# Kernel tuning notes

Measured on AMD Instinct MI355X. Metric: run time of the kernel, lower is better.

## Reference

```python
import jax, jax.numpy as jnp
import numpy as np

B, N, M, T = 64, 1024, 32, 25
R, SO, SA, H, OD = 512, 512, 256, 8, 10

def _ln(x, g, b):
    mu = x.mean(-1, keepdims=True)
    v = ((x - mu) ** 2).mean(-1, keepdims=True)
    return (x - mu) / jnp.sqrt(v + 1e-5) * g + b

def _glu(x):
    a, g = jnp.split(x, 2, axis=-1)
    return a * jax.nn.sigmoid(g)

def setup_inputs() -> dict:
    key = jax.random.key(0)
    ks = jax.random.split(key, 64)
    it = iter(range(64))
    def rn(shape, s=0.05):
        return jax.random.normal(ks[next(it)], shape, jnp.float32) * s
    def zr(shape):
        return jnp.zeros(shape, jnp.float32)
    def on(shape):
        return jnp.ones(shape, jnp.float32)
    inp = dict(
        x=jax.random.normal(ks[next(it)], (B, 1, 28, 28), jnp.float32),
        start_activated_state=rn((N,)),
        start_trace=rn((N, M)),
        ie_w1=rn((128, 784)), ie_b1=zr(128), ie_g1=on(128), ie_bn1=zr(128),
        ie_w2=rn((64, 128)), ie_b2=zr(64), ie_g2=on(64), ie_bn2=zr(64),
        ie_w3=rn((R, 64)), ie_b3=zr(R),
        kv_w=rn((R, R)), kv_b=zr(R), kv_g=on(R), kv_bn=zr(R),
        q_w=rn((R, SA)), q_b=zr(R),
        in_proj_w=rn((3 * R, R)), in_proj_b=zr(3 * R),
        out_proj_w=rn((R, R)), out_proj_b=zr(R),
        syn_w=rn((2 * N, R + N)), syn_b=zr(2 * N), syn_g=on(N), syn_bn=zr(N),
        nlm_w1=rn((N, M, 256)), nlm_b1=zr((N, 256)),
        nlm_w2=rn((N, 128)), nlm_b2=zr(N),
        decay_action=zr(SA), decay_out=zr(SO),
        op_w1=rn((256, SO)), op_b1=zr(256), op_g1=on(256), op_bn1=zr(256),
        op_w2=rn((64, 256)), op_b2=zr(64), op_g2=on(64), op_bn2=zr(64),
        op_w3=rn((OD, 64)), op_b3=zr(OD),
        idx_out_l=jax.random.randint(ks[next(it)], (SO,), 0, N, jnp.int32),
        idx_out_r=jax.random.randint(ks[next(it)], (SO,), 0, N, jnp.int32),
        idx_act_l=jax.random.randint(ks[next(it)], (SA,), 0, N, jnp.int32),
        idx_act_r=jax.random.randint(ks[next(it)], (SA,), 0, N, jnp.int32),
    )
    return inp

def reference(x, start_activated_state, start_trace,
              ie_w1, ie_b1, ie_g1, ie_bn1, ie_w2, ie_b2, ie_g2, ie_bn2, ie_w3, ie_b3,
              kv_w, kv_b, kv_g, kv_bn, q_w, q_b,
              in_proj_w, in_proj_b, out_proj_w, out_proj_b,
              syn_w, syn_b, syn_g, syn_bn,
              nlm_w1, nlm_b1, nlm_w2, nlm_b2,
              decay_action, decay_out,
              op_w1, op_b1, op_g1, op_bn1, op_w2, op_b2, op_g2, op_bn2, op_w3, op_b3,
              idx_out_l, idx_out_r, idx_act_l, idx_act_r):
    Bx = x.shape[0]
    f = x.reshape(Bx, -1)  # [B,784]
    h = jax.nn.relu(_ln(f @ ie_w1.T + ie_b1, ie_g1, ie_bn1))
    h = jax.nn.relu(_ln(h @ ie_w2.T + ie_b2, ie_g2, ie_bn2))
    enc = h @ ie_w3.T + ie_b3                       # [B,R]
    kv = _ln(enc @ kv_w.T + kv_b, kv_g, kv_bn)      # [B,R]; single kv token
    # MultiheadAttention with kv_len == 1: softmax over a single key is exactly 1,
    # so attn_out = out_proj(Wv @ kv + bv) regardless of the query (q_proj of
    # sync_action has no effect on the output). Hoisted out of the tick loop.
    Wv = in_proj_w[2 * R:]
    bv = in_proj_b[2 * R:]
    attn_out = (kv @ Wv.T + bv) @ out_proj_w.T + out_proj_b  # [B,R]
    rA = jnp.exp(-jnp.clip(decay_action, 0.0, 15.0))  # [SA]
    rO = jnp.exp(-jnp.clip(decay_out, 0.0, 15.0))     # [SO]
    act0 = jnp.broadcast_to(start_activated_state, (Bx, N))
    trace0 = jnp.broadcast_to(start_trace, (Bx, N, M))
    # pre-loop 'out' sync init: alpha = z_i*z_j, beta = 1
    aO0 = act0[:, idx_out_l] * act0[:, idx_out_r]
    bO0 = jnp.ones_like(aO0)
    # 'action' sync starts from None; recurrence from (0,0) reproduces it exactly
    aA0 = jnp.zeros((Bx, SA), x.dtype)
    bA0 = jnp.zeros((Bx, SA), x.dtype)
    log_od = np.log(float(OD)).astype(np.float32)

    def step(carry, _):
        trace, act, aA, bA, aO, bO = carry
        ppA = act[:, idx_act_l] * act[:, idx_act_r]
        aA = rA * aA + ppA
        bA = rA * bA + 1.0
        # sync_action -> q_proj -> attention query: no effect on output (see above)
        pre = jnp.concatenate([attn_out, act], axis=-1)          # [B,R+N]
        ns = _ln(_glu(pre @ syn_w.T + syn_b), syn_g, syn_bn)     # [B,N]
        trace = jnp.concatenate([trace[:, :, 1:], ns[:, :, None]], axis=-1)  # [B,N,M]
        # batched per-neuron NLMs: Linear(M,256) -> GLU -> Linear(128,1)
        hh = _glu(jnp.einsum('bnm,nmh->bnh', trace, nlm_w1) + nlm_b1)  # [B,N,128]
        act = jnp.einsum('bnh,nh->bn', hh, nlm_w2) + nlm_b2            # [B,N]
        ppO = act[:, idx_out_l] * act[:, idx_out_r]
        aO = rO * aO + ppO
        bO = rO * bO + 1.0
        syncO = aO / jnp.sqrt(bO + 1e-8)
        p = jax.nn.relu(_ln(syncO @ op_w1.T + op_b1, op_g1, op_bn1))
        p = jax.nn.relu(_ln(p @ op_w2.T + op_b2, op_g2, op_bn2))
        pred = p @ op_w3.T + op_b3                                # [B,OD]
        probs = jax.nn.softmax(pred, axis=-1)
        ent = -jnp.sum(probs * jnp.log(probs + 1e-10), axis=-1) / log_od
        cert = jnp.stack([ent, 1.0 - ent], axis=-1)               # [B,2]
        return (trace, act, aA, bA, aO, bO), (pred, cert)

    _, (preds, certs) = jax.lax.scan(step, (trace0, act0, aA0, bA0, aO0, bO0), None, length=T)
    predictions = jnp.moveaxis(preds, 0, -1)   # [B,OD,T]
    certainties = jnp.moveaxis(certs, 0, -1)   # [B,2,T]
    return predictions, certainties
```

## Files before the change

### kernel.cpp

```cpp
#include <hip/hip_runtime.h>
#include <math.h>

#define TRW 57
#define TRN (TRW * 64)

__device__ __forceinline__ float wave_sum(float v) {
  #pragma unroll
  for (int off = 32; off; off >>= 1) v += __shfl_xor(v, off, 64);
  return v;
}

template<int NT>
__device__ __forceinline__ float2 block_sum2(float a, float b, float2* sh) {
  constexpr int NW = NT / 64;
  a = wave_sum(a); b = wave_sum(b);
  int w = threadIdx.x >> 6, l = threadIdx.x & 63;
  if (l == 0) sh[w] = make_float2(a, b);
  __syncthreads();
  float2 r = make_float2(0.f, 0.f);
  #pragma unroll
  for (int i = 0; i < NW; i++) { r.x += sh[i].x; r.y += sh[i].y; }
  __syncthreads();
  return r;
}

__device__ __forceinline__ float sigmoidf(float x) {
  return 1.f / (1.f + expf(-x));
}

__global__ __launch_bounds__(512) void k_enc(const float* __restrict__ x,
    const float* __restrict__ w1, const float* __restrict__ b1,
    const float* __restrict__ g1, const float* __restrict__ bn1,
    const float* __restrict__ w2, const float* __restrict__ b2,
    const float* __restrict__ g2, const float* __restrict__ bn2,
    const float* __restrict__ w3, const float* __restrict__ b3,
    const float* __restrict__ kvw, const float* __restrict__ kvb,
    const float* __restrict__ kvg, const float* __restrict__ kvbn,
    const float* __restrict__ ipw, const float* __restrict__ ipb,
    const float* __restrict__ opw, const float* __restrict__ opb,
    float* __restrict__ attn) {
  int b = blockIdx.x, tid = threadIdx.x, w = tid >> 6, l = tid & 63;
  __shared__ float xs[784];
  __shared__ float A[512];
  __shared__ float Bv[512];
  __shared__ float buf1[128];
  __shared__ float buf2[64];
  __shared__ float2 sh[8];
  for (int i = tid; i < 784; i += 512) xs[i] = x[b * 784 + i];
  __syncthreads();
  for (int r = 0; r < 16; r++) {
    int o = r * 8 + w;
    float s = 0.f;
    for (int k = l; k < 784; k += 64) s += xs[k] * w1[o * 784 + k];
    s = wave_sum(s);
    if (l == 0) buf1[o] = s + b1[o];
  }
  __syncthreads();
  {
    float v = (tid < 128) ? buf1[tid] : 0.f;
    float2 s2 = block_sum2<512>(v, v * v, sh);
    if (tid < 128) {
      float mu = s2.x * (1.f / 128.f), var = s2.y * (1.f / 128.f) - mu * mu;
      buf1[tid] = fmaxf((v - mu) * rsqrtf(var + 1e-5f) * g1[tid] + bn1[tid], 0.f);
    }
  }
  __syncthreads();
  for (int r = 0; r < 8; r++) {
    int o = r * 8 + w;
    float s = buf1[l] * w2[o * 128 + l] + buf1[l + 64] * w2[o * 128 + l + 64];
    s = wave_sum(s);
    if (l == 0) buf2[o] = s + b2[o];
  }
  __syncthreads();
  if (tid < 64) {
    float v = buf2[tid];
    float sa = wave_sum(v), sb = wave_sum(v * v);
    float mu = sa * (1.f / 64.f), var = sb * (1.f / 64.f) - mu * mu;
    buf2[tid] = fmaxf((v - mu) * rsqrtf(var + 1e-5f) * g2[tid] + bn2[tid], 0.f);
  }
  __syncthreads();
  for (int r = 0; r < 64; r++) {
    int o = r * 8 + w;
    float s = wave_sum(buf2[l] * w3[o * 64 + l]);
    if (l == 0) A[o] = s + b3[o];
  }
  __syncthreads();
  for (int r = 0; r < 64; r++) {
    int o = r * 8 + w;
    float s = 0.f;
    #pragma unroll
    for (int k = 0; k < 8; k++) s += A[l + 64 * k] * kvw[o * 512 + l + 64 * k];
    s = wave_sum(s);
    if (l == 0) Bv[o] = s + kvb[o];
  }
  __syncthreads();
  {
    float v = Bv[tid];
    float2 s2 = block_sum2<512>(v, v * v, sh);
    float mu = s2.x * (1.f / 512.f), var = s2.y * (1.f / 512.f) - mu * mu;
    Bv[tid] = (v - mu) * rsqrtf(var + 1e-5f) * kvg[tid] + kvbn[tid];
  }
  __syncthreads();
  for (int r = 0; r < 64; r++) {
    int o = r * 8 + w;
    float s = 0.f;
    #pragma unroll
    for (int k = 0; k < 8; k++) s += Bv[l + 64 * k] * ipw[(1024 + o) * 512 + l + 64 * k];
    s = wave_sum(s);
    if (l == 0) A[o] = s + ipb[1024 + o];
  }
  __syncthreads();
  for (int r = 0; r < 64; r++) {
    int o = r * 8 + w;
    float s = 0.f;
    #pragma unroll
    for (int k = 0; k < 8; k++) s += A[l + 64 * k] * opw[o * 512 + l + 64 * k];
    s = wave_sum(s);
    if (l == 0) attn[b * 512 + o] = s + opb[o];
  }
}

__global__ void k_setup(const float* __restrict__ st, const float* __restrict__ sas,
                        const int* __restrict__ il, const int* __restrict__ ir,
                        const float* __restrict__ opw1, const float* __restrict__ opw2,
                        float* __restrict__ trace, float* __restrict__ act,
                        float* __restrict__ aO, float* __restrict__ bO,
                        float* __restrict__ w1t, float* __restrict__ w2t) {
  long i = (long)blockIdx.x * 256 + threadIdx.x;
  if (i < 2097152) {
    int b = (int)(i & 63), j = (int)((i >> 6) & 31), n = (int)(i >> 11);
    trace[n * TRN + j * 64 + b] = st[n * 32 + j];
    return;
  }
  i -= 2097152;
  if (i < 65536) {
    act[i] = sas[i & 1023];
    return;
  }
  i -= 65536;
  if (i < 32768) {
    int o = (int)(i & 511);
    aO[i] = sas[il[o]] * sas[ir[o]];
    bO[i] = 1.f;
    return;
  }
  i -= 32768;
  if (i < 131072) {
    int o = (int)(i & 255), k = (int)(i >> 8);
    w1t[i] = opw1[o * 512 + k];
    return;
  }
  i -= 131072;
  if (i < 16384) {
    int o = (int)(i & 63), k = (int)(i >> 6);
    w2t[i] = opw2[o * 256 + k];
  }
}

__device__ void op_body(int b, int t, const float* __restrict__ act,
                        const float* __restrict__ decay,
                        const int* __restrict__ il, const int* __restrict__ ir,
                        float* __restrict__ aO, float* __restrict__ bO,
                        const float* __restrict__ w1t, const float* __restrict__ bb1,
                        const float* __restrict__ g1, const float* __restrict__ bn1,
                        const float* __restrict__ w2t, const float* __restrict__ bb2,
                        const float* __restrict__ g2, const float* __restrict__ bn2,
                        const float* __restrict__ w3, const float* __restrict__ bb3,
                        float* __restrict__ out,
                        float* so, float* p1s, float* qred, float* p2s,
                        float* preds, float2* sh) {
  int tid = threadIdx.x;
  #pragma unroll
  for (int r = 0; r < 2; r++) {
    int o = r * 256 + tid;
    float rr = expf(-fminf(fmaxf(decay[o], 0.f), 15.f));
    float pp = act[b * 1024 + il[o]] * act[b * 1024 + ir[o]];
    float a = rr * aO[b * 512 + o] + pp;
    float bbv = rr * bO[b * 512 + o] + 1.f;
    aO[b * 512 + o] = a;
    bO[b * 512 + o] = bbv;
    so[o] = a * rsqrtf(bbv + 1e-8f);
  }
  __syncthreads();
  float p = bb1[tid];
  #pragma unroll 8
  for (int k = 0; k < 512; k++) p += so[k] * w1t[k * 256 + tid];
  float2 s = block_sum2<256>(p, p * p, sh);
  {
    float mu = s.x * (1.f / 256.f), var = s.y * (1.f / 256.f) - mu * mu;
    p1s[tid] = fmaxf((p - mu) * rsqrtf(var + 1e-5f) * g1[tid] + bn1[tid], 0.f);
  }
  __syncthreads();
  {
    int o = tid & 63, tg = tid >> 6;
    float q = 0.f;
    #pragma unroll 4
    for (int j = 0; j < 64; j++) {
      int k = tg * 64 + j;
      q += p1s[k] * w2t[k * 64 + o];
    }
    qred[tid] = q;
  }
  __syncthreads();
  if (tid < 64) {
    float p2 = qred[tid] + qred[tid + 64] + qred[tid + 128] + qred[tid + 192] + bb2[tid];
    float sa = wave_sum(p2), sb = wave_sum(p2 * p2);
    float mu = sa * (1.f / 64.f), var = sb * (1.f / 64.f) - mu * mu;
    float y = (p2 - mu) * rsqrtf(var + 1e-5f) * g2[tid] + bn2[tid];
    p2s[tid] = fmaxf(y, 0.f);
  }
  __syncthreads();
  if (tid < 160) {
    int o = tid >> 4, j = tid & 15;
    const float* w3r = w3 + o * 64 + j * 4;
    const float* pp2 = p2s + j * 4;
    float sv = w3r[0] * pp2[0] + w3r[1] * pp2[1] + w3r[2] * pp2[2] + w3r[3] * pp2[3];
    #pragma unroll
    for (int off = 8; off; off >>= 1) sv += __shfl_xor(sv, off, 64);
    if (j == 0) {
      float pr = sv + bb3[o];
      preds[o] = pr;
      out[b * 250 + o * 25 + t] = pr;
    }
  }
  __syncthreads();
  if (tid == 0) {
    float mx = preds[0];
    #pragma unroll
    for (int k = 1; k < 10; k++) mx = fmaxf(mx, preds[k]);
    float sum = 0.f, e[10];
    #pragma unroll
    for (int k = 0; k < 10; k++) { e[k] = expf(preds[k] - mx); sum += e[k]; }
    float ent = 0.f;
    #pragma unroll
    for (int k = 0; k < 10; k++) {
      float pr = e[k] / sum;
      ent -= pr * logf(pr + 1e-10f);
    }
    ent *= (1.f / 2.302585093f);
    out[16000 + b * 50 + t] = ent;
    out[16000 + b * 50 + 25 + t] = 1.f - ent;
  }
}

__global__ __launch_bounds__(256) void k_F(const float* __restrict__ attn,
    const float* __restrict__ act, const float* __restrict__ synw,
    float* __restrict__ part,
    const float* __restrict__ decay, const int* __restrict__ il, const int* __restrict__ ir,
    float* __restrict__ aO, float* __restrict__ bO,
    const float* __restrict__ w1t, const float* __restrict__ bb1,
    const float* __restrict__ g1, const float* __restrict__ bn1,
    const float* __restrict__ w2t, const float* __restrict__ bb2,
    const float* __restrict__ g2, const float* __restrict__ bn2,
    const float* __restrict__ w3, const float* __restrict__ bb3,
    float* __restrict__ out, int t) {
  __shared__ __align__(16) float pre_t[32 * 68];
  __shared__ __align__(16) float w_lds[32 * 68];
  __shared__ __align__(16) float so[512];
  __shared__ float p1s[256];
  __shared__ float qred[256];
  __shared__ float p2s[64];
  __shared__ float preds[10];
  __shared__ float2 sh[4];
  int bid = blockIdx.x;
  if (bid >= 512) {
    if (t > 0)
      op_body(bid - 512, t - 1, act, decay, il, ir, aO, bO, w1t, bb1, g1, bn1,
              w2t, bb2, g2, bn2, w3, bb3, out, so, p1s, qred, p2s, preds, sh);
    return;
  }
  int ct = bid & 31;
  int kc = bid >> 5;
  int tid = threadIdx.x;
  int tb = tid >> 4, tc = tid & 15;
  int b0 = tb * 4, c0 = tc * 4;
  float acc[4][4];
  #pragma unroll
  for (int i = 0; i < 4; i++)
    #pragma unroll
    for (int j = 0; j < 4; j++) acc[i][j] = 0.f;

  for (int kt = 0; kt < 96; kt += 32) {
    int k0 = kc * 96 + kt;
    #pragma unroll
    for (int r = 0; r < 8; r++) {
      int idx = r * 256 + tid;
      int kk = idx & 31;
      int bb = idx >> 5;
      int kg = k0 + kk;
      float pv = (kg < 512) ? attn[bb * 512 + kg] : act[bb * 1024 + (kg - 512)];
      pre_t[kk * 68 + bb] = pv;
      w_lds[kk * 68 + bb] = synw[(ct * 64 + bb) * 1536 + kg];
    }
    __syncthreads();
    #pragma unroll 8
    for (int kk = 0; kk < 32; kk++) {
      float4 av = *(const float4*)(pre_t + kk * 68 + b0);
      float4 wv = *(const float4*)(w_lds + kk * 68 + c0);
      float a[4] = {av.x, av.y, av.z, av.w};
      float w[4] = {wv.x, wv.y, wv.z, wv.w};
      #pragma unroll
      for (int i = 0; i < 4; i++)
        #pragma unroll
        for (int j = 0; j < 4; j++) acc[i][j] += a[i] * w[j];
    }
    __syncthreads();
  }
  float* pb = part + kc * (64 * 2048);
  #pragma unroll
  for (int i = 0; i < 4; i++) {
    float4 st4 = make_float4(acc[i][0], acc[i][1], acc[i][2], acc[i][3]);
    *(float4*)(pb + (b0 + i) * 2048 + ct * 64 + c0) = st4;
  }
}

__global__ __launch_bounds__(256) void k_op_tail(const float* __restrict__ act,
    const float* __restrict__ decay, const int* __restrict__ il, const int* __restrict__ ir,
    float* __restrict__ aO, float* __restrict__ bO,
    const float* __restrict__ w1t, const float* __restrict__ bb1,
    const float* __restrict__ g1, const float* __restrict__ bn1,
    const float* __restrict__ w2t, const float* __restrict__ bb2,
    const float* __restrict__ g2, const float* __restrict__ bn2,
    const float* __restrict__ w3, const float* __restrict__ bb3,
    float* __restrict__ out) {
  __shared__ __align__(16) float so[512];
  __shared__ float p1s[256];
  __shared__ float qred[256];
  __shared__ float p2s[64];
  __shared__ float preds[10];
  __shared__ float2 sh[4];
  op_body(blockIdx.x, 24, act, decay, il, ir, aO, bO, w1t, bb1, g1, bn1,
          w2t, bb2, g2, bn2, w3, bb3, out, so, p1s, qred, p2s, preds, sh);
}

__global__ __launch_bounds__(1024) void k_syn_ln(const float* __restrict__ part,
                                                 const float* __restrict__ synb,
                                                 const float* __restrict__ sg,
                                                 const float* __restrict__ sbn,
                                                 float* __restrict__ ns) {
  __shared__ float2 sh[16];
  int b = blockIdx.x, n = threadIdx.x;
  float a = synb[n], g = synb[n + 1024];
  #pragma unroll
  for (int kc = 0; kc < 16; kc++) {
    const float* pb = part + kc * (64 * 2048) + b * 2048;
    a += pb[n];
    g += pb[n + 1024];
  }
  float val = a * sigmoidf(g);
  float2 s = block_sum2<1024>(val, val * val, sh);
  float mu = s.x * (1.f / 1024.f);
  float var = s.y * (1.f / 1024.f) - mu * mu;
  ns[b * 1024 + n] = (val - mu) * rsqrtf(var + 1e-5f) * sg[n] + sbn[n];
}

__global__ __launch_bounds__(256) void k_nlm(const float* __restrict__ trace_c,
                                             float* __restrict__ trace,
                                             const float* __restrict__ ns,
                                             const float* __restrict__ w1,
                                             const float* __restrict__ b1,
                                             const float* __restrict__ w2,
                                             const float* __restrict__ b2,
                                             float* __restrict__ act, int t) {
  int n = blockIdx.x;
  int tid = threadIdx.x;
  int tb = tid >> 5;
  int tjj = tid & 31;
  __shared__ __align__(16) float At[32 * 68];
  __shared__ __align__(16) float w1s[32 * 256];
  __shared__ float b1s[256];
  __shared__ float w2s[128];

  const float4* tw4 = (const float4*)(trace_c + n * TRN + (t + 1) * 64);
  #pragma unroll
  for (int r = 0; r < 2; r++) {
    int idx = r * 256 + tid;
    if (idx < 496) {
      float4 f4 = tw4[idx];
      int fo = idx * 4;
      int m = fo >> 6, bb = fo & 63;
      *(float4*)(At + m * 68 + bb) = f4;
    }
  }
  if (tid < 64) {
    float v = ns[tid * 1024 + n];
    At[31 * 68 + tid] = v;
    trace[n * TRN + (32 + t) * 64 + tid] = v;
  }
  const float4* w1n = (const float4*)(w1 + n * 8192);
  float4* w1s4 = (float4*)w1s;
  #pragma unroll
  for (int r = 0; r < 8; r++) w1s4[r * 256 + tid] = w1n[r * 256 + tid];
  b1s[tid] = b1[n * 256 + tid];
  if (tid < 128) w2s[tid] = w2[n * 128 + tid];
  __syncthreads();

  float h[8][8];
  #pragma unroll
  for (int jj = 0; jj < 8; jj++) {
    float bv = b1s[tjj + 32 * jj];
    #pragma unroll
    for (int i = 0; i < 8; i++) h[i][jj] = bv;
  }
  for (int m = 0; m < 32; m++) {
    float4 a0 = *(const float4*)(At + m * 68 + tb * 8);
    float4 a1 = *(const float4*)(At + m * 68 + tb * 8 + 4);
    float a[8] = {a0.x, a0.y, a0.z, a0.w, a1.x, a1.y, a1.z, a1.w};
    float w[8];
    #pragma unroll
    for (int jj = 0; jj < 8; jj++) w[jj] = w1s[m * 256 + tjj + 32 * jj];
    #pragma unroll
    for (int i = 0; i < 8; i++)
      #pragma unroll
      for (int jj = 0; jj < 8; jj++) h[i][jj] += a[i] * w[jj];
  }
  float b2n = b2[n];
  #pragma unroll
  for (int i = 0; i < 8; i++) {
    float p = 0.f;
    #pragma unroll
    for (int jj = 0; jj < 4; jj++) {
      float hh = h[i][jj] * sigmoidf(h[i][jj + 4]);
      p += hh * w2s[tjj + 32 * jj];
    }
    #pragma unroll
    for (int off = 16; off > 0; off >>= 1) p += __shfl_xor(p, off, 64);
    if (tjj == 0) act[(tb * 8 + i) * 1024 + n] = p + b2n;
  }
}

extern "C" void kernel_launch(void* const* d_in, const int* in_sizes, int n_in,
                              void* d_out, int out_size, void* d_ws, size_t ws_size,
                              hipStream_t stream) {
  const float* x        = (const float*)d_in[0];
  const float* sas      = (const float*)d_in[1];
  const float* st       = (const float*)d_in[2];
  const float* ie_w1    = (const float*)d_in[3];
  const float* ie_b1    = (const float*)d_in[4];
  const float* ie_g1    = (const float*)d_in[5];
  const float* ie_bn1   = (const float*)d_in[6];
  const float* ie_w2    = (const float*)d_in[7];
  const float* ie_b2    = (const float*)d_in[8];
  const float* ie_g2    = (const float*)d_in[9];
  const float* ie_bn2   = (const float*)d_in[10];
  const float* ie_w3    = (const float*)d_in[11];
  const float* ie_b3    = (const float*)d_in[12];
  const float* kv_w     = (const float*)d_in[13];
  const float* kv_b     = (const float*)d_in[14];
  const float* kv_g     = (const float*)d_in[15];
  const float* kv_bn    = (const float*)d_in[16];
  const float* ip_w     = (const float*)d_in[19];
  const float* ip_b     = (const float*)d_in[20];
  const float* op_w     = (const float*)d_in[21];
  const float* op_b     = (const float*)d_in[22];
  const float* syn_w    = (const float*)d_in[23];
  const float* syn_b    = (const float*)d_in[24];
  const float* syn_g    = (const float*)d_in[25];
  const float* syn_bn   = (const float*)d_in[26];
  const float* nlm_w1   = (const float*)d_in[27];
  const float* nlm_b1   = (const float*)d_in[28];
  const float* nlm_w2   = (const float*)d_in[29];
  const float* nlm_b2   = (const float*)d_in[30];
  const float* decay_o  = (const float*)d_in[32];
  const float* op_w1    = (const float*)d_in[33];
  const float* op_b1    = (const float*)d_in[34];
  const float* op_g1    = (const float*)d_in[35];
  const float* op_bn1   = (const float*)d_in[36];
  const float* op_w2    = (const float*)d_in[37];
  const float* op_b2    = (const float*)d_in[38];
  const float* op_g2    = (const float*)d_in[39];
  const float* op_bn2   = (const float*)d_in[40];
  const float* op_w3    = (const float*)d_in[41];
  const float* op_b3    = (const float*)d_in[42];
  const int* idx_ol     = (const int*)d_in[43];
  const int* idx_or     = (const int*)d_in[44];

  float* out = (float*)d_out;
  float* ws = (float*)d_ws;
  float* attn  = ws;
  float* act   = attn + 32768;
  float* aO    = act + 65536;
  float* bO    = aO + 32768;
  float* ns    = bO + 32768;
  float* w1t   = ns + 65536;
  float* w2t   = w1t + 131072;
  float* part  = w2t + 16384;
  float* trace = part + 2097152;

  k_enc<<<64, 512, 0, stream>>>(x, ie_w1, ie_b1, ie_g1, ie_bn1,
                                ie_w2, ie_b2, ie_g2, ie_bn2, ie_w3, ie_b3,
                                kv_w, kv_b, kv_g, kv_bn, ip_w, ip_b, op_w, op_b, attn);
  k_setup<<<9152, 256, 0, stream>>>(st, sas, idx_ol, idx_or, op_w1, op_w2,
                                    trace, act, aO, bO, w1t, w2t);

  for (int t = 0; t < 25; t++) {
    k_F<<<576, 256, 0, stream>>>(attn, act, syn_w, part,
                                 decay_o, idx_ol, idx_or, aO, bO,
                                 w1t, op_b1, op_g1, op_bn1,
                                 w2t, op_b2, op_g2, op_bn2,
                                 op_w3, op_b3, out, t);
    k_syn_ln<<<64, 1024, 0, stream>>>(part, syn_b, syn_g, syn_bn, ns);
    k_nlm<<<1024, 256, 0, stream>>>(trace, trace, ns, nlm_w1, nlm_b1,
                                    nlm_w2, nlm_b2, act, t);
  }
  k_op_tail<<<64, 256, 0, stream>>>(act, decay_o, idx_ol, idx_or, aO, bO,
                                    w1t, op_b1, op_g1, op_bn1,
                                    w2t, op_b2, op_g2, op_bn2,
                                    op_w3, op_b3, out);
}
```

Before: 1.944 ms.

## Transpose encoder weights in setup and compute one output per thread

k_setup now also transposes the input-encoder, kv, value-projection and out-projection weights into a k-blocked float4 layout, stored in the scratch buffer that k_F later reuses. k_enc is rewritten so each thread computes one output neuron with coalesced float4 weight loads and inputs broadcast from shared memory. This replaces the old wave-per-output dot products with their shuffle reductions. The cost is extra transpose work and weight traffic in setup, and k_enc must now run after k_setup.

Result: faster. 1.714 ms (-11.8%).

```diff
diff --git a/kernel.cpp b/kernel.cpp
--- a/kernel.cpp
+++ b/kernel.cpp
@@ -29,103 +29,134 @@
 }
 
 __global__ __launch_bounds__(512) void k_enc(const float* __restrict__ x,
-    const float* __restrict__ w1, const float* __restrict__ b1,
+    const float* __restrict__ w1te, const float* __restrict__ b1,
     const float* __restrict__ g1, const float* __restrict__ bn1,
-    const float* __restrict__ w2, const float* __restrict__ b2,
+    const float* __restrict__ w2te, const float* __restrict__ b2,
     const float* __restrict__ g2, const float* __restrict__ bn2,
-    const float* __restrict__ w3, const float* __restrict__ b3,
-    const float* __restrict__ kvw, const float* __restrict__ kvb,
+    const float* __restrict__ w3te, const float* __restrict__ b3,
+    const float* __restrict__ kvwt, const float* __restrict__ kvb,
     const float* __restrict__ kvg, const float* __restrict__ kvbn,
-    const float* __restrict__ ipw, const float* __restrict__ ipb,
-    const float* __restrict__ opw, const float* __restrict__ opb,
+    const float* __restrict__ vwt, const float* __restrict__ ipb,
+    const float* __restrict__ opwt, const float* __restrict__ opb,
     float* __restrict__ attn) {
-  int b = blockIdx.x, tid = threadIdx.x, w = tid >> 6, l = tid & 63;
+  int b = blockIdx.x, tid = threadIdx.x;
   __shared__ float xs[784];
-  __shared__ float A[512];
-  __shared__ float Bv[512];
-  __shared__ float buf1[128];
-  __shared__ float buf2[64];
+  __shared__ float h1[128];
+  __shared__ float h2[64];
+  __shared__ float enc[512];
+  __shared__ float red[512];
   __shared__ float2 sh[8];
   for (int i = tid; i < 784; i += 512) xs[i] = x[b * 784 + i];
   __syncthreads();
-  for (int r = 0; r < 16; r++) {
-    int o = r * 8 + w;
-    float s = 0.f;
-    for (int k = l; k < 784; k += 64) s += xs[k] * w1[o * 784 + k];
-    s = wave_sum(s);
-    if (l == 0) buf1[o] = s + b1[o];
-  }
-  __syncthreads();
-  {
-    float v = (tid < 128) ? buf1[tid] : 0.f;
-    float2 s2 = block_sum2<512>(v, v * v, sh);
+  {
+    int tg = tid >> 7, o = tid & 127;
+    const float4* wp = (const float4*)w1te;
+    float s0 = 0.f, s1 = 0.f, s2 = 0.f, s3 = 0.f;
+    int kb0 = tg * 49;
+    #pragma unroll 7
+    for (int j = 0; j < 49; j++) {
+      int kb = kb0 + j;
+      float4 w4 = wp[kb * 128 + o];
+      int k = kb * 4;
+      s0 += xs[k] * w4.x; s1 += xs[k + 1] * w4.y;
+      s2 += xs[k + 2] * w4.z; s3 += xs[k + 3] * w4.w;
+    }
+    red[tid] = (s0 + s1) + (s2 + s3);
+    __syncthreads();
+    float v = 0.f;
+    if (tid < 128)
+      v = red[tid] + red[tid + 128] + red[tid + 256] + red[tid + 384] + b1[tid];
+    float2 s2v = block_sum2<512>(tid < 128 ? v : 0.f, tid < 128 ? v * v : 0.f, sh);
     if (tid < 128) {
-      float mu = s2.x * (1.f / 128.f), var = s2.y * (1.f / 128.f) - mu * mu;
-      buf1[tid] = fmaxf((v - mu) * rsqrtf(var + 1e-5f) * g1[tid] + bn1[tid], 0.f);
-    }
-  }
-  __syncthreads();
-  for (int r = 0; r < 8; r++) {
-    int o = r * 8 + w;
-    float s = buf1[l] * w2[o * 128 + l] + buf1[l + 64] * w2[o * 128 + l + 64];
-    s = wave_sum(s);
-    if (l == 0) buf2[o] = s + b2[o];
+      float mu = s2v.x * (1.f / 128.f), var = s2v.y * (1.f / 128.f) - mu * mu;
+      h1[tid] = fmaxf((v - mu) * rsqrtf(var + 1e-5f) * g1[tid] + bn1[tid], 0.f);
+    }
   }
   __syncthreads();
   if (tid < 64) {
-    float v = buf2[tid];
-    float sa = wave_sum(v), sb = wave_sum(v * v);
+    const float4* wp = (const float4*)w2te;
+    float s0 = 0.f, s1 = 0.f, s2 = 0.f, s3 = 0.f;
+    #pragma unroll 8
+    for (int kb = 0; kb < 32; kb++) {
+      float4 w4 = wp[kb * 64 + tid];
+      int k = kb * 4;
+      s0 += h1[k] * w4.x; s1 += h1[k + 1] * w4.y;
+      s2 += h1[k + 2] * w4.z; s3 += h1[k + 3] * w4.w;
+    }
+    float s = (s0 + s1) + (s2 + s3) + b2[tid];
+    float sa = wave_sum(s), sb = wave_sum(s * s);
     float mu = sa * (1.f / 64.f), var = sb * (1.f / 64.f) - mu * mu;
-    buf2[tid] = fmaxf((v - mu) * rsqrtf(var + 1e-5f) * g2[tid] + bn2[tid], 0.f);
-  }
-  __syncthreads();
-  for (int r = 0; r < 64; r++) {
-    int o = r * 8 + w;
-    float s = wave_sum(buf2[l] * w3[o * 64 + l]);
-    if (l == 0) A[o] = s + b3[o];
-  }
-  __syncthreads();
-  for (int r = 0; r < 64; r++) {
-    int o = r * 8 + w;
-    float s = 0.f;
-    #pragma unroll
-    for (int k = 0; k < 8; k++) s += A[l + 64 * k] * kvw[o * 512 + l + 64 * k];
-    s = wave_sum(s);
-    if (l == 0) Bv[o] = s + kvb[o];
-  }
-  __syncthreads();
-  {
-    float v = Bv[tid];
-    float2 s2 = block_sum2<512>(v, v * v, sh);
-    float mu = s2.x * (1.f / 512.f), var = s2.y * (1.f / 512.f) - mu * mu;
-    Bv[tid] = (v - mu) * rsqrtf(var + 1e-5f) * kvg[tid] + kvbn[tid];
-  }
-  __syncthreads();
-  for (int r = 0; r < 64; r++) {
-    int o = r * 8 + w;
-    float s = 0.f;
-    #pragma unroll
-    for (int k = 0; k < 8; k++) s += Bv[l + 64 * k] * ipw[(1024 + o) * 512 + l + 64 * k];
-    s = wave_sum(s);
-    if (l == 0) A[o] = s + ipb[1024 + o];
-  }
-  __syncthreads();
-  for (int r = 0; r < 64; r++) {
-    int o = r * 8 + w;
-    float s = 0.f;
-    #pragma unroll
-    for (int k = 0; k < 8; k++) s += A[l + 64 * k] * opw[o * 512 + l + 64 * k];
-    s = wave_sum(s);
-    if (l == 0) attn[b * 512 + o] = s + opb[o];
+    h2[tid] = fmaxf((s - mu) * rsqrtf(var + 1e-5f) * g2[tid] + bn2[tid], 0.f);
+  }
+  __syncthreads();
+  {
+    const float4* wp = (const float4*)w3te;
+    float s0 = 0.f, s1 = 0.f, s2 = 0.f, s3 = 0.f;
+    #pragma unroll 8
+    for (int kb = 0; kb < 16; kb++) {
+      float4 w4 = wp[kb * 512 + tid];
+      int k = kb * 4;
+      s0 += h2[k] * w4.x; s1 += h2[k + 1] * w4.y;
+      s2 += h2[k + 2] * w4.z; s3 += h2[k + 3] * w4.w;
+    }
+    enc[tid] = (s0 + s1) + (s2 + s3) + b3[tid];
+  }
+  __syncthreads();
+  {
+    const float4* wp = (const float4*)kvwt;
+    float s0 = 0.f, s1 = 0.f, s2 = 0.f, s3 = 0.f;
+    #pragma unroll 8
+    for (int kb = 0; kb < 128; kb++) {
+      float4 w4 = wp[kb * 512 + tid];
+      int k = kb * 4;
+      s0 += enc[k] * w4.x; s1 += enc[k + 1] * w4.y;
+      s2 += enc[k + 2] * w4.z; s3 += enc[k + 3] * w4.w;
+    }
+    float s = (s0 + s1) + (s2 + s3) + kvb[tid];
+    float2 s2v = block_sum2<512>(s, s * s, sh);
+    float mu = s2v.x * (1.f / 512.f), var = s2v.y * (1.f / 512.f) - mu * mu;
+    red[tid] = (s - mu) * rsqrtf(var + 1e-5f) * kvg[tid] + kvbn[tid];
+  }
+  __syncthreads();
+  {
+    const float4* wp = (const float4*)vwt;
+    float s0 = 0.f, s1 = 0.f, s2 = 0.f, s3 = 0.f;
+    #pragma unroll 8
+    for (int kb = 0; kb < 128; kb++) {
+      float4 w4 = wp[kb * 512 + tid];
+      int k = kb * 4;
+      s0 += red[k] * w4.x; s1 += red[k + 1] * w4.y;
+      s2 += red[k + 2] * w4.z; s3 += red[k + 3] * w4.w;
+    }
+    enc[tid] = (s0 + s1) + (s2 + s3) + ipb[1024 + tid];
+  }
+  __syncthreads();
+  {
+    const float4* wp = (const float4*)opwt;
+    float s0 = 0.f, s1 = 0.f, s2 = 0.f, s3 = 0.f;
+    #pragma unroll 8
+    for (int kb = 0; kb < 128; kb++) {
+      float4 w4 = wp[kb * 512 + tid];
+      int k = kb * 4;
+      s0 += enc[k] * w4.x; s1 += enc[k + 1] * w4.y;
+      s2 += enc[k + 2] * w4.z; s3 += enc[k + 3] * w4.w;
+    }
+    attn[b * 512 + tid] = (s0 + s1) + (s2 + s3) + opb[tid];
   }
 }
 
 __global__ void k_setup(const float* __restrict__ st, const float* __restrict__ sas,
                         const int* __restrict__ il, const int* __restrict__ ir,
                         const float* __restrict__ opw1, const float* __restrict__ opw2,
+                        const float* __restrict__ iew1, const float* __restrict__ iew2,
+                        const float* __restrict__ iew3, const float* __restrict__ kvw,
+                        const float* __restrict__ ipw, const float* __restrict__ opw,
                         float* __restrict__ trace, float* __restrict__ act,
                         float* __restrict__ aO, float* __restrict__ bO,
-                        float* __restrict__ w1t, float* __restrict__ w2t) {
+                        float* __restrict__ w1t, float* __restrict__ w2t,
+                        float* __restrict__ w1te, float* __restrict__ w2te,
+                        float* __restrict__ w3te, float* __restrict__ kvwt,
+                        float* __restrict__ vwt, float* __restrict__ opwt) {
   long i = (long)blockIdx.x * 256 + threadIdx.x;
   if (i < 2097152) {
     int b = (int)(i & 63), j = (int)((i >> 6) & 31), n = (int)(i >> 11);
@@ -154,6 +185,42 @@
   if (i < 16384) {
     int o = (int)(i & 63), k = (int)(i >> 6);
     w2t[i] = opw2[o * 256 + k];
+    return;
+  }
+  i -= 16384;
+  if (i < 100352) {
+    int kk = (int)(i & 3), o = (int)((i >> 2) & 127), kb = (int)(i >> 9);
+    w1te[i] = iew1[o * 784 + kb * 4 + kk];
+    return;
+  }
+  i -= 100352;
+  if (i < 8192) {
+    int kk = (int)(i & 3), o = (int)((i >> 2) & 63), kb = (int)(i >> 8);
+    w2te[i] = iew2[o * 128 + kb * 4 + kk];
+    return;
+  }
+  i -= 8192;
+  if (i < 32768) {
+    int kk = (int)(i & 3), o = (int)((i >> 2) & 511), kb = (int)(i >> 11);
+    w3te[i] = iew3[o * 64 + kb * 4 + kk];
+    return;
+  }
+  i -= 32768;
+  if (i < 262144) {
+    int kk = (int)(i & 3), o = (int)((i >> 2) & 511), kb = (int)(i >> 11);
+    kvwt[i] = kvw[o * 512 + kb * 4 + kk];
+    return;
+  }
+  i -= 262144;
+  if (i < 262144) {
+    int kk = (int)(i & 3), o = (int)((i >> 2) & 511), kb = (int)(i >> 11);
+    vwt[i] = ipw[(1024 + o) * 512 + kb * 4 + kk];
+    return;
+  }
+  i -= 262144;
+  if (i < 262144) {
+    int kk = (int)(i & 3), o = (int)((i >> 2) & 511), kb = (int)(i >> 11);
+    opwt[i] = opw[o * 512 + kb * 4 + kk];
   }
 }
 
@@ -487,11 +554,21 @@
   float* part  = w2t + 16384;
   float* trace = part + 2097152;
 
-  k_enc<<<64, 512, 0, stream>>>(x, ie_w1, ie_b1, ie_g1, ie_bn1,
-                                ie_w2, ie_b2, ie_g2, ie_bn2, ie_w3, ie_b3,
-                                kv_w, kv_b, kv_g, kv_bn, ip_w, ip_b, op_w, op_b, attn);
-  k_setup<<<9152, 256, 0, stream>>>(st, sas, idx_ol, idx_or, op_w1, op_w2,
-                                    trace, act, aO, bO, w1t, w2t);
+  float* w1te = part;
+  float* w2te = w1te + 100352;
+  float* w3te = w2te + 8192;
+  float* kvwt = w3te + 32768;
+  float* vwt  = kvwt + 262144;
+  float* opwt = vwt + 262144;
+
+  k_setup<<<12776, 256, 0, stream>>>(st, sas, idx_ol, idx_or, op_w1, op_w2,
+                                     ie_w1, ie_w2, ie_w3, kv_w, ip_w, op_w,
+                                     trace, act, aO, bO, w1t, w2t,
+                                     w1te, w2te, w3te, kvwt, vwt, opwt);
+  k_enc<<<64, 512, 0, stream>>>(x, w1te, ie_b1, ie_g1, ie_bn1,
+                                w2te, ie_b2, ie_g2, ie_bn2, w3te, ie_b3,
+                                kvwt, kv_b, kv_g, kv_bn, vwt, ip_b,
+                                opwt, op_b, attn);
 
   for (int t = 0; t < 25; t++) {
     k_F<<<576, 256, 0, stream>>>(attn, act, syn_w, part,
```
